# Kernel optimization log

Measured on AMD Instinct MI355X. Metric: run time of the kernel, lower is better.

The kernel has to match this reference:

```python
import jax, jax.numpy as jnp
import numpy as np

N = 16384          # num users / nodes
INPUT_SIZE = 4096  # num items
EMB = 500
E = 524288         # num edges (avg degree 32)


def setup_inputs() -> dict:
    key = jax.random.key(0)
    ks = jax.random.split(key, 8)
    x = jax.random.uniform(ks[0], (N, INPUT_SIZE), dtype=jnp.float32)
    edge_index = jax.random.randint(ks[1], (2, E), 0, N, dtype=jnp.int64)
    # kaiming-uniform-ish init for enc/dec weights
    bound_enc = 1.0 / np.sqrt(INPUT_SIZE)
    wenc = jax.random.uniform(ks[2], (EMB, INPUT_SIZE), jnp.float32, -bound_enc, bound_enc)
    benc = jax.random.uniform(ks[3], (EMB,), jnp.float32, -bound_enc, bound_enc)
    bound_dec = 1.0 / np.sqrt(EMB)
    wdec = jax.random.uniform(ks[4], (INPUT_SIZE, EMB), jnp.float32, -bound_dec, bound_dec)
    bdec = jax.random.uniform(ks[5], (INPUT_SIZE,), jnp.float32, -bound_dec, bound_dec)
    conv_weight = jax.random.normal(ks[6], (1,), jnp.float32) * 0.01
    return {"x": x, "edge_index": edge_index, "wenc": wenc, "benc": benc,
            "wdec": wdec, "bdec": bdec, "conv_weight": conv_weight}


def graph_conv0d(h_in, edge_index, weight):
    # GCN-style symmetric norm with unit edge weights, then scatter-add propagate.
    row, col = edge_index[0], edge_index[1]
    n = h_in.shape[0]
    ew = jnp.ones((edge_index.shape[1],), dtype=h_in.dtype)
    deg = jax.ops.segment_sum(ew, row, num_segments=n)          # [N]
    dinv = jnp.where(deg > 0, jax.lax.rsqrt(jnp.maximum(deg, 1e-30)), 0.0)
    norm = dinv[row] * dinv[col]                                 # [E]
    h = h_in * weight                                            # scalar gate
    msg = norm[:, None] * h[row]                                 # gather sources
    aggr = jax.ops.segment_sum(msg, col, num_segments=n)         # scatter to targets
    return aggr + h_in                                           # update: residual


def reference(x, edge_index, wenc, benc, wdec, bdec, conv_weight):
    # dropout layers are identity in eval mode
    h = jax.nn.sigmoid(x @ wenc.T + benc)        # [N, EMB] encode
    h = graph_conv0d(h, edge_index, conv_weight) # GCN propagate
    p = h @ wdec.T + bdec                        # [N, INPUT_SIZE] decode
    return p
```

## Files before the change

kernel.cpp:

```cpp
#include <hip/hip_runtime.h>
#include <hip/hip_bf16.h>
#include <stdint.h>

#define N_NODES 16384
#define IN_SIZE 4096
#define EMB 500
#define EMBP 512
#define NEDGE 524288

typedef __attribute__((ext_vector_type(8))) short bf16x8_t;
typedef __attribute__((ext_vector_type(4))) float f32x4_t;

__device__ __forceinline__ unsigned short f2bf(float f) {
    union { float f; unsigned u; } v; v.f = f;
    unsigned r = v.u + 0x7FFFu + ((v.u >> 16) & 1u);
    return (unsigned short)(r >> 16);
}
__device__ __forceinline__ float bf2f(unsigned short h) {
    union { float f; unsigned u; } v; v.u = ((unsigned)h) << 16;
    return v.f;
}

__device__ __forceinline__ void gload_lds16(const void* g, void* l) {
    __builtin_amdgcn_global_load_lds(
        (__attribute__((address_space(1))) void*)(g),
        (__attribute__((address_space(3))) void*)(l),
        16, 0, 0);
}

__global__ void zero_i32(int* p, int n) {
    int i = blockIdx.x * 256 + threadIdx.x;
    if (i < n) p[i] = 0;
}

__global__ void hist_k(const int* __restrict__ ei, int* __restrict__ deg, int* __restrict__ coldeg) {
    int e = blockIdx.x * 256 + threadIdx.x;
    int r = ei[e];
    int c = ei[NEDGE + e];
    atomicAdd(&deg[r], 1);
    atomicAdd(&coldeg[c], 1);
}

__global__ void dinv_k(const int* __restrict__ deg, float* __restrict__ dinv) {
    int i = blockIdx.x * 256 + threadIdx.x;
    int d = deg[i];
    dinv[i] = d > 0 ? rsqrtf((float)d) : 0.f;
}

__global__ void scan_k(const int* __restrict__ coldeg, int* __restrict__ colptr, int* __restrict__ cursor) {
    __shared__ int part[256];
    int t = threadIdx.x;
    int base = t * 64;
    int s = 0;
    for (int i = 0; i < 64; ++i) s += coldeg[base + i];
    part[t] = s;
    __syncthreads();
    for (int off = 1; off < 256; off <<= 1) {
        int v = part[t];
        int add = (t >= off) ? part[t - off] : 0;
        __syncthreads();
        part[t] = v + add;
        __syncthreads();
    }
    int ex = (t > 0) ? part[t - 1] : 0;
    for (int i = 0; i < 64; ++i) {
        colptr[base + i] = ex;
        cursor[base + i] = ex;
        ex += coldeg[base + i];
    }
    if (t == 255) colptr[N_NODES] = ex;
}

__global__ void fill_k(const int* __restrict__ ei, const float* __restrict__ dinv,
                       int* __restrict__ cursor, int* __restrict__ csr_src, float* __restrict__ csr_nrm) {
    int e = blockIdx.x * 256 + threadIdx.x;
    int r = ei[e];
    int c = ei[NEDGE + e];
    int pos = atomicAdd(&cursor[c], 1);
    csr_src[pos] = r;
    csr_nrm[pos] = dinv[r] * dinv[c];
}

__global__ void cast_wenc_k(const float* __restrict__ w, unsigned short* __restrict__ wb) {
    int i = blockIdx.x * 256 + threadIdx.x;
    int row = i >> 12;
    wb[i] = (row < EMB) ? f2bf(w[i]) : (unsigned short)0;
}

__global__ void cast_wdec_k(const float* __restrict__ w, unsigned short* __restrict__ wb) {
    int i = blockIdx.x * 256 + threadIdx.x;
    int row = i >> 9;
    int col = i & 511;
    wb[i] = (col < EMB) ? f2bf(w[row * EMB + col]) : (unsigned short)0;
}

template<bool AF32, bool SIG>
__global__ __launch_bounds__(256, 2) void gemm_bt(
    const void* __restrict__ Av, const unsigned short* __restrict__ B,
    const float* __restrict__ bias, void* __restrict__ Cout,
    int M, int N, int K, int NL)
{
    constexpr int BM = 128, BN = 128, BK = 32;
    __shared__ unsigned short As[BM * BK];
    __shared__ unsigned short Bs[BN * BK];
    int tid = threadIdx.x;
    int lane = tid & 63;
    int wave = tid >> 6;
    int rowA0 = blockIdx.x * BM;
    int colB0 = blockIdx.y * BN;
    int wm = (wave >> 1) * 64;
    int wn = (wave & 1) * 64;

    f32x4_t acc[4][4];
    #pragma unroll
    for (int i = 0; i < 4; ++i)
        #pragma unroll
        for (int j = 0; j < 4; ++j)
            acc[i][j] = (f32x4_t){0.f, 0.f, 0.f, 0.f};

    int fr = lane & 15;
    int kb = (lane >> 4) * 8;

    int sRow = wave * 32 + (lane >> 2);
    int sCol = (lane & 3) * 8;
    const unsigned short* Ab = (const unsigned short*)Av;
    unsigned short* AsW = &As[(wave * 32) * BK];
    unsigned short* BsW = &Bs[(wave * 32) * BK];

    int cr = tid >> 3;
    int ck = (tid & 7) * 4;

    for (int k0 = 0; k0 < K; k0 += BK) {
        __syncthreads();
        if constexpr (AF32) {
            const float* A = (const float*)Av;
            #pragma unroll
            for (int rep = 0; rep < 4; ++rep) {
                float4 v = *(const float4*)(A + (size_t)(rowA0 + cr + rep * 32) * K + k0 + ck);
                uint2 pv;
                pv.x = (unsigned)f2bf(v.x) | ((unsigned)f2bf(v.y) << 16);
                pv.y = (unsigned)f2bf(v.z) | ((unsigned)f2bf(v.w) << 16);
                *(uint2*)&As[(cr + rep * 32) * BK + ck] = pv;
            }
        } else {
            #pragma unroll
            for (int t = 0; t < 2; ++t)
                gload_lds16(Ab + (size_t)(rowA0 + sRow + t * 16) * K + k0 + sCol,
                            AsW + t * 16 * BK);
        }
        #pragma unroll
        for (int t = 0; t < 2; ++t)
            gload_lds16(B + (size_t)(colB0 + sRow + t * 16) * K + k0 + sCol,
                        BsW + t * 16 * BK);
        __syncthreads();

        bf16x8_t af[4], bfr[4];
        #pragma unroll
        for (int i = 0; i < 4; ++i)
            af[i] = *(const bf16x8_t*)&As[(wm + i * 16 + fr) * BK + kb];
        #pragma unroll
        for (int j = 0; j < 4; ++j)
            bfr[j] = *(const bf16x8_t*)&Bs[(wn + j * 16 + fr) * BK + kb];
        #pragma unroll
        for (int i = 0; i < 4; ++i)
            #pragma unroll
            for (int j = 0; j < 4; ++j)
                acc[i][j] = __builtin_amdgcn_mfma_f32_16x16x32_bf16(af[i], bfr[j], acc[i][j], 0, 0, 0);
    }

    int cl = lane & 15;
    int rq = (lane >> 4) * 4;
    #pragma unroll
    for (int j = 0; j < 4; ++j) {
        int col = colB0 + wn + j * 16 + cl;
        float b = (col < NL) ? bias[col] : 0.f;
        #pragma unroll
        for (int i = 0; i < 4; ++i) {
            #pragma unroll
            for (int rr = 0; rr < 4; ++rr) {
                int row = rowA0 + wm + i * 16 + rq + rr;
                float v = acc[i][j][rr] + b;
                if constexpr (SIG) {
                    v = 1.f / (1.f + __expf(-v));
                    unsigned short o = (col < NL) ? f2bf(v) : (unsigned short)0;
                    ((unsigned short*)Cout)[(size_t)row * N + col] = o;
                } else {
                    ((float*)Cout)[(size_t)row * N + col] = v;
                }
            }
        }
    }
}

__global__ __launch_bounds__(256) void aggregate_k(
    const unsigned short* __restrict__ h, const int* __restrict__ colptr,
    const int* __restrict__ csr_src, const float* __restrict__ csr_nrm,
    const float* __restrict__ convw, unsigned short* __restrict__ h2)
{
    int lane = threadIdx.x & 63;
    int node = blockIdx.x * 4 + (threadIdx.x >> 6);
    float cw = convw[0];
    float acc[8] = {0.f, 0.f, 0.f, 0.f, 0.f, 0.f, 0.f, 0.f};
    int p0 = colptr[node], p1 = colptr[node + 1];
    int off = lane * 8;
    for (int i = p0; i < p1; ++i) {
        int r = csr_src[i];
        float w = csr_nrm[i] * cw;
        uint4 hv = *(const uint4*)(h + (size_t)r * EMBP + off);
        const unsigned short* hs = (const unsigned short*)&hv;
        #pragma unroll
        for (int j = 0; j < 8; ++j) acc[j] += w * bf2f(hs[j]);
    }
    uint4 hn = *(const uint4*)(h + (size_t)node * EMBP + off);
    const unsigned short* hs = (const unsigned short*)&hn;
    uint4 o;
    unsigned short ov[8];
    #pragma unroll
    for (int j = 0; j < 8; ++j) ov[j] = f2bf(acc[j] + bf2f(hs[j]));
    o.x = (unsigned)ov[0] | ((unsigned)ov[1] << 16);
    o.y = (unsigned)ov[2] | ((unsigned)ov[3] << 16);
    o.z = (unsigned)ov[4] | ((unsigned)ov[5] << 16);
    o.w = (unsigned)ov[6] | ((unsigned)ov[7] << 16);
    *(uint4*)(h2 + (size_t)node * EMBP + off) = o;
}

extern "C" void kernel_launch(void* const* d_in, const int* in_sizes, int n_in,
                              void* d_out, int out_size, void* d_ws, size_t ws_size,
                              hipStream_t stream) {
    const float* x = (const float*)d_in[0];
    const int* ei = (const int*)d_in[1];
    const float* wenc = (const float*)d_in[2];
    const float* benc = (const float*)d_in[3];
    const float* wdec = (const float*)d_in[4];
    const float* bdec = (const float*)d_in[5];
    const float* convw = (const float*)d_in[6];
    float* out = (float*)d_out;

    char* ws = (char*)d_ws;
    size_t off = 0;
    auto alloc = [&](size_t bytes) -> void* {
        void* p = ws + off;
        off += (bytes + 255) & ~(size_t)255;
        return p;
    };
    unsigned short* wencb = (unsigned short*)alloc((size_t)EMBP * IN_SIZE * 2);
    unsigned short* wdecb = (unsigned short*)alloc((size_t)IN_SIZE * EMBP * 2);
    unsigned short* h     = (unsigned short*)alloc((size_t)N_NODES * EMBP * 2);
    unsigned short* h2    = (unsigned short*)alloc((size_t)N_NODES * EMBP * 2);
    int*   deg     = (int*)alloc(N_NODES * 4);
    int*   coldeg  = (int*)alloc(N_NODES * 4);
    float* dinv    = (float*)alloc(N_NODES * 4);
    int*   colptr  = (int*)alloc((N_NODES + 1) * 4);
    int*   cursor  = (int*)alloc(N_NODES * 4);
    int*   csr_src = (int*)alloc((size_t)NEDGE * 4);
    float* csr_nrm = (float*)alloc((size_t)NEDGE * 4);

    zero_i32<<<(2 * N_NODES) / 256, 256, 0, stream>>>(deg, 2 * N_NODES);
    hist_k<<<NEDGE / 256, 256, 0, stream>>>(ei, deg, coldeg);
    dinv_k<<<N_NODES / 256, 256, 0, stream>>>(deg, dinv);
    scan_k<<<1, 256, 0, stream>>>(coldeg, colptr, cursor);
    fill_k<<<NEDGE / 256, 256, 0, stream>>>(ei, dinv, cursor, csr_src, csr_nrm);
    cast_wenc_k<<<(EMBP * IN_SIZE) / 256, 256, 0, stream>>>(wenc, wencb);
    cast_wdec_k<<<(IN_SIZE * EMBP) / 256, 256, 0, stream>>>(wdec, wdecb);

    gemm_bt<true, true><<<dim3(N_NODES / 128, EMBP / 128), 256, 0, stream>>>(
        x, wencb, benc, h, N_NODES, EMBP, IN_SIZE, EMB);
    aggregate_k<<<N_NODES / 4, 256, 0, stream>>>(h, colptr, csr_src, csr_nrm, convw, h2);
    gemm_bt<false, false><<<dim3(N_NODES / 128, IN_SIZE / 128), 256, 0, stream>>>(
        h2, wdecb, bdec, out, N_NODES, IN_SIZE, EMBP, IN_SIZE);
}
```

Baseline: 840.4 us.

## Load fp32 A tiles directly to LDS and convert at fragment read, widen BK to 64

```diff
diff --git a/kernel.cpp b/kernel.cpp
--- a/kernel.cpp
+++ b/kernel.cpp
@@ -19,6 +19,22 @@
 __device__ __forceinline__ float bf2f(unsigned short h) {
     union { float f; unsigned u; } v; v.u = ((unsigned)h) << 16;
     return v.f;
+}
+
+__device__ __forceinline__ unsigned pkbf2(float a, float b) {
+    union { __hip_bfloat162 h; unsigned u; } c;
+    c.h = __float22bfloat162_rn(float2{a, b});
+    return c.u;
+}
+__device__ __forceinline__ bf16x8_t cvt8(const float* p) {
+    f32x4_t lo = *(const f32x4_t*)p;
+    f32x4_t hi = *(const f32x4_t*)(p + 4);
+    union { bf16x8_t v; unsigned u[4]; } r;
+    r.u[0] = pkbf2(lo[0], lo[1]);
+    r.u[1] = pkbf2(lo[2], lo[3]);
+    r.u[2] = pkbf2(hi[0], hi[1]);
+    r.u[3] = pkbf2(hi[2], hi[3]);
+    return r.v;
 }
 
 __device__ __forceinline__ void gload_lds16(const void* g, void* l) {
@@ -94,78 +110,92 @@
     wb[i] = (col < EMB) ? f2bf(w[row * EMB + col]) : (unsigned short)0;
 }
 
-template<bool AF32, bool SIG>
-__global__ __launch_bounds__(256, 2) void gemm_bt(
+template<int BM, bool AF32, bool SIG>
+__global__ __launch_bounds__(256, 4) void gemm_bt(
     const void* __restrict__ Av, const unsigned short* __restrict__ B,
     const float* __restrict__ bias, void* __restrict__ Cout,
     int M, int N, int K, int NL)
 {
-    constexpr int BM = 128, BN = 128, BK = 32;
-    __shared__ unsigned short As[BM * BK];
-    __shared__ unsigned short Bs[BN * BK];
+    constexpr int BN = 128, BK = 64;
+    constexpr int MI = BM / 32;
+    constexpr int ABYTES = AF32 ? 4 : 2;
+    __shared__ __align__(16) char AsRaw[BM * BK * ABYTES];
+    __shared__ __align__(16) char BsRaw[BN * BK * 2];
+
     int tid = threadIdx.x;
     int lane = tid & 63;
     int wave = tid >> 6;
     int rowA0 = blockIdx.x * BM;
     int colB0 = blockIdx.y * BN;
-    int wm = (wave >> 1) * 64;
+    int wm = (wave >> 1) * (BM / 2);
     int wn = (wave & 1) * 64;
 
-    f32x4_t acc[4][4];
+    f32x4_t acc[MI][4];
     #pragma unroll
-    for (int i = 0; i < 4; ++i)
+    for (int i = 0; i < MI; ++i)
         #pragma unroll
         for (int j = 0; j < 4; ++j)
             acc[i][j] = (f32x4_t){0.f, 0.f, 0.f, 0.f};
 
     int fr = lane & 15;
     int kb = (lane >> 4) * 8;
-
-    int sRow = wave * 32 + (lane >> 2);
-    int sCol = (lane & 3) * 8;
-    const unsigned short* Ab = (const unsigned short*)Av;
-    unsigned short* AsW = &As[(wave * 32) * BK];
-    unsigned short* BsW = &Bs[(wave * 32) * BK];
-
-    int cr = tid >> 3;
-    int ck = (tid & 7) * 4;
 
     for (int k0 = 0; k0 < K; k0 += BK) {
         __syncthreads();
         if constexpr (AF32) {
             const float* A = (const float*)Av;
-            #pragma unroll
-            for (int rep = 0; rep < 4; ++rep) {
-                float4 v = *(const float4*)(A + (size_t)(rowA0 + cr + rep * 32) * K + k0 + ck);
-                uint2 pv;
-                pv.x = (unsigned)f2bf(v.x) | ((unsigned)f2bf(v.y) << 16);
-                pv.y = (unsigned)f2bf(v.z) | ((unsigned)f2bf(v.w) << 16);
-                *(uint2*)&As[(cr + rep * 32) * BK + ck] = pv;
+            float* AsF = (float*)AsRaw;
+            int r = wave * 16 + (lane >> 4);
+            int c = (lane & 15) * 4;
+            #pragma unroll
+            for (int t = 0; t < 4; ++t)
+                gload_lds16(A + (size_t)(rowA0 + r + t * 4) * K + k0 + c,
+                            AsF + (wave * 16 + t * 4) * BK);
+        } else {
+            const unsigned short* A = (const unsigned short*)Av;
+            unsigned short* AsU = (unsigned short*)AsRaw;
+            int r = wave * 32 + (lane >> 3);
+            int c = (lane & 7) * 8;
+            #pragma unroll
+            for (int t = 0; t < 4; ++t)
+                gload_lds16(A + (size_t)(rowA0 + r + t * 8) * K + k0 + c,
+                            AsU + (wave * 32 + t * 8) * BK);
+        }
+        {
+            unsigned short* BsU = (unsigned short*)BsRaw;
+            int r = wave * 32 + (lane >> 3);
+            int c = (lane & 7) * 8;
+            #pragma unroll
+            for (int t = 0; t < 4; ++t)
+                gload_lds16(B + (size_t)(colB0 + r + t * 8) * K + k0 + c,
+                            BsU + (wave * 32 + t * 8) * BK);
+        }
+        __syncthreads();
+
+        #pragma unroll
+        for (int ks = 0; ks < 2; ++ks) {
+            bf16x8_t af[MI], bfr[4];
+            if constexpr (AF32) {
+                const float* AsF = (const float*)AsRaw;
+                #pragma unroll
+                for (int i = 0; i < MI; ++i)
+                    af[i] = cvt8(AsF + (wm + i * 16 + fr) * BK + ks * 32 + kb);
+            } else {
+                const unsigned short* AsU = (const unsigned short*)AsRaw;
+                #pragma unroll
+                for (int i = 0; i < MI; ++i)
+                    af[i] = *(const bf16x8_t*)&AsU[(wm + i * 16 + fr) * BK + ks * 32 + kb];
             }
-        } else {
-            #pragma unroll
-            for (int t = 0; t < 2; ++t)
-                gload_lds16(Ab + (size_t)(rowA0 + sRow + t * 16) * K + k0 + sCol,
-                            AsW + t * 16 * BK);
+            const unsigned short* BsU = (const unsigned short*)BsRaw;
+            #pragma unroll
+            for (int j = 0; j < 4; ++j)
+                bfr[j] = *(const bf16x8_t*)&BsU[(wn + j * 16 + fr) * BK + ks * 32 + kb];
+            #pragma unroll
+            for (int i = 0; i < MI; ++i)
+                #pragma unroll
+                for (int j = 0; j < 4; ++j)
+                    acc[i][j] = __builtin_amdgcn_mfma_f32_16x16x32_bf16(af[i], bfr[j], acc[i][j], 0, 0, 0);
         }
-        #pragma unroll
-        for (int t = 0; t < 2; ++t)
-            gload_lds16(B + (size_t)(colB0 + sRow + t * 16) * K + k0 + sCol,
-                        BsW + t * 16 * BK);
-        __syncthreads();
-
-        bf16x8_t af[4], bfr[4];
-        #pragma unroll
-        for (int i = 0; i < 4; ++i)
-            af[i] = *(const bf16x8_t*)&As[(wm + i * 16 + fr) * BK + kb];
-        #pragma unroll
-        for (int j = 0; j < 4; ++j)
-            bfr[j] = *(const bf16x8_t*)&Bs[(wn + j * 16 + fr) * BK + kb];
-        #pragma unroll
-        for (int i = 0; i < 4; ++i)
-            #pragma unroll
-            for (int j = 0; j < 4; ++j)
-                acc[i][j] = __builtin_amdgcn_mfma_f32_16x16x32_bf16(af[i], bfr[j], acc[i][j], 0, 0, 0);
     }
 
     int cl = lane & 15;
@@ -175,7 +205,7 @@
         int col = colB0 + wn + j * 16 + cl;
         float b = (col < NL) ? bias[col] : 0.f;
         #pragma unroll
-        for (int i = 0; i < 4; ++i) {
+        for (int i = 0; i < MI; ++i) {
             #pragma unroll
             for (int rr = 0; rr < 4; ++rr) {
                 int row = rowA0 + wm + i * 16 + rq + rr;
@@ -263,9 +293,9 @@
     cast_wenc_k<<<(EMBP * IN_SIZE) / 256, 256, 0, stream>>>(wenc, wencb);
     cast_wdec_k<<<(IN_SIZE * EMBP) / 256, 256, 0, stream>>>(wdec, wdecb);
 
-    gemm_bt<true, true><<<dim3(N_NODES / 128, EMBP / 128), 256, 0, stream>>>(
+    gemm_bt<64, true, true><<<dim3(N_NODES / 64, EMBP / 128), 256, 0, stream>>>(
         x, wencb, benc, h, N_NODES, EMBP, IN_SIZE, EMB);
     aggregate_k<<<N_NODES / 4, 256, 0, stream>>>(h, colptr, csr_src, csr_nrm, convw, h2);
-    gemm_bt<false, false><<<dim3(N_NODES / 128, IN_SIZE / 128), 256, 0, stream>>>(
+    gemm_bt<128, false, false><<<dim3(N_NODES / 128, IN_SIZE / 128), 256, 0, stream>>>(
         h2, wdecb, bdec, out, N_NODES, IN_SIZE, EMBP, IN_SIZE);
 }
```

Measured after the change: 849.4 us. Within noise of the previous version (+1.1%).

## Stream fp32 A tiles directly to LDS with XOR swizzle and unroll aggregation

Applied to the files above, without the earlier changes.

```diff
diff --git a/kernel.cpp b/kernel.cpp
--- a/kernel.cpp
+++ b/kernel.cpp
@@ -19,6 +19,12 @@
 __device__ __forceinline__ float bf2f(unsigned short h) {
     union { float f; unsigned u; } v; v.u = ((unsigned)h) << 16;
     return v.f;
+}
+
+__device__ __forceinline__ unsigned pkbf2(float a, float b) {
+    union { __hip_bfloat162 h; unsigned u; } c;
+    c.h = __float22bfloat162_rn(float2{a, b});
+    return c.u;
 }
 
 __device__ __forceinline__ void gload_lds16(const void* g, void* l) {
@@ -95,14 +101,16 @@
 }
 
 template<bool AF32, bool SIG>
-__global__ __launch_bounds__(256, 2) void gemm_bt(
+__global__ __launch_bounds__(256, 4) void gemm_bt(
     const void* __restrict__ Av, const unsigned short* __restrict__ B,
     const float* __restrict__ bias, void* __restrict__ Cout,
     int M, int N, int K, int NL)
 {
     constexpr int BM = 128, BN = 128, BK = 32;
-    __shared__ unsigned short As[BM * BK];
-    __shared__ unsigned short Bs[BN * BK];
+    constexpr int ABYTES = AF32 ? 4 : 2;
+    __shared__ __align__(16) char AsRaw[BM * BK * ABYTES];
+    __shared__ __align__(16) unsigned short Bs[BN * BK];
+
     int tid = threadIdx.x;
     int lane = tid & 63;
     int wave = tid >> 6;
@@ -119,48 +127,62 @@
             acc[i][j] = (f32x4_t){0.f, 0.f, 0.f, 0.f};
 
     int fr = lane & 15;
-    int kb = (lane >> 4) * 8;
-
-    int sRow = wave * 32 + (lane >> 2);
-    int sCol = (lane & 3) * 8;
-    const unsigned short* Ab = (const unsigned short*)Av;
-    unsigned short* AsW = &As[(wave * 32) * BK];
-    unsigned short* BsW = &Bs[(wave * 32) * BK];
-
-    int cr = tid >> 3;
-    int ck = (tid & 7) * 4;
+    int g  = lane >> 4;
+
+    int r16 = lane >> 2;
+    int c4  = lane & 3;
+    int sColB = (c4 ^ ((r16 >> 1) & 3)) * 8;
+    int r8  = lane >> 3;
+    int c8  = lane & 7;
+    int sColA32 = (c8 ^ (r8 & 7)) * 4;
 
     for (int k0 = 0; k0 < K; k0 += BK) {
         __syncthreads();
         if constexpr (AF32) {
             const float* A = (const float*)Av;
+            float* AsF = (float*)AsRaw;
             #pragma unroll
-            for (int rep = 0; rep < 4; ++rep) {
-                float4 v = *(const float4*)(A + (size_t)(rowA0 + cr + rep * 32) * K + k0 + ck);
-                uint2 pv;
-                pv.x = (unsigned)f2bf(v.x) | ((unsigned)f2bf(v.y) << 16);
-                pv.y = (unsigned)f2bf(v.z) | ((unsigned)f2bf(v.w) << 16);
-                *(uint2*)&As[(cr + rep * 32) * BK + ck] = pv;
-            }
+            for (int t = 0; t < 4; ++t)
+                gload_lds16(A + (size_t)(rowA0 + wave * 32 + t * 8 + r8) * K + k0 + sColA32,
+                            AsF + (wave * 32 + t * 8) * BK);
         } else {
+            const unsigned short* A = (const unsigned short*)Av;
+            unsigned short* AsU = (unsigned short*)AsRaw;
             #pragma unroll
             for (int t = 0; t < 2; ++t)
-                gload_lds16(Ab + (size_t)(rowA0 + sRow + t * 16) * K + k0 + sCol,
-                            AsW + t * 16 * BK);
+                gload_lds16(A + (size_t)(rowA0 + wave * 32 + t * 16 + r16) * K + k0 + sColB,
+                            AsU + (wave * 32 + t * 16) * BK);
         }
         #pragma unroll
         for (int t = 0; t < 2; ++t)
-            gload_lds16(B + (size_t)(colB0 + sRow + t * 16) * K + k0 + sCol,
-                        BsW + t * 16 * BK);
+            gload_lds16(B + (size_t)(colB0 + wave * 32 + t * 16 + r16) * K + k0 + sColB,
+                        Bs + (wave * 32 + t * 16) * BK);
         __syncthreads();
 
         bf16x8_t af[4], bfr[4];
         #pragma unroll
-        for (int i = 0; i < 4; ++i)
-            af[i] = *(const bf16x8_t*)&As[(wm + i * 16 + fr) * BK + kb];
-        #pragma unroll
-        for (int j = 0; j < 4; ++j)
-            bfr[j] = *(const bf16x8_t*)&Bs[(wn + j * 16 + fr) * BK + kb];
+        for (int i = 0; i < 4; ++i) {
+            int row = wm + i * 16 + fr;
+            if constexpr (AF32) {
+                const float* AsF = (const float*)AsRaw;
+                f32x4_t lo = *(const f32x4_t*)&AsF[row * BK + (((2 * g)     ^ (fr & 7)) * 4)];
+                f32x4_t hi = *(const f32x4_t*)&AsF[row * BK + (((2 * g + 1) ^ (fr & 7)) * 4)];
+                union { bf16x8_t v; unsigned u[4]; } rr;
+                rr.u[0] = pkbf2(lo[0], lo[1]);
+                rr.u[1] = pkbf2(lo[2], lo[3]);
+                rr.u[2] = pkbf2(hi[0], hi[1]);
+                rr.u[3] = pkbf2(hi[2], hi[3]);
+                af[i] = rr.v;
+            } else {
+                const unsigned short* AsU = (const unsigned short*)AsRaw;
+                af[i] = *(const bf16x8_t*)&AsU[row * BK + ((g ^ ((fr >> 1) & 3)) * 8)];
+            }
+        }
+        #pragma unroll
+        for (int j = 0; j < 4; ++j) {
+            int row = wn + j * 16 + fr;
+            bfr[j] = *(const bf16x8_t*)&Bs[row * BK + ((g ^ ((fr >> 1) & 3)) * 8)];
+        }
         #pragma unroll
         for (int i = 0; i < 4; ++i)
             #pragma unroll
@@ -203,7 +225,18 @@
     float acc[8] = {0.f, 0.f, 0.f, 0.f, 0.f, 0.f, 0.f, 0.f};
     int p0 = colptr[node], p1 = colptr[node + 1];
     int off = lane * 8;
-    for (int i = p0; i < p1; ++i) {
+    int i = p0;
+    for (; i + 1 < p1; i += 2) {
+        int r0 = csr_src[i], r1 = csr_src[i + 1];
+        float w0 = csr_nrm[i] * cw, w1 = csr_nrm[i + 1] * cw;
+        uint4 v0 = *(const uint4*)(h + (size_t)r0 * EMBP + off);
+        uint4 v1 = *(const uint4*)(h + (size_t)r1 * EMBP + off);
+        const unsigned short* s0 = (const unsigned short*)&v0;
+        const unsigned short* s1 = (const unsigned short*)&v1;
+        #pragma unroll
+        for (int j = 0; j < 8; ++j) acc[j] += w0 * bf2f(s0[j]) + w1 * bf2f(s1[j]);
+    }
+    if (i < p1) {
         int r = csr_src[i];
         float w = csr_nrm[i] * cw;
         uint4 hv = *(const uint4*)(h + (size_t)r * EMBP + off);
```

After: 838.9 us. Within noise of the previous version (-0.2%).
